# Kernel tuning notes

Measured on AMD Instinct MI355X. Metric: run time of the kernel, lower is better.

## Reference

```python
import jax, jax.numpy as jnp
import numpy as np

B, NP, DL, DA, H, NB = 8, 81920, 16, 4, 128, 3
DT_TOTAL = DL + DA  # 20
NSTEPS = 4
DT = 0.1


def setup_inputs() -> dict:
    key = jax.random.key(0)
    k1, k2, k3, k4 = jax.random.split(key, 4)
    inputs = jax.random.normal(k1, (B, NP, DT_TOTAL), dtype=jnp.float32)
    neighbours = jax.random.randint(k2, (NP, NB), 0, NP, dtype=jnp.int64)
    fan_in = NB * DT_TOTAL  # 60
    W1 = jax.random.normal(k3, (fan_in, H), dtype=jnp.float32) / np.sqrt(fan_in)
    b1 = jnp.zeros((H,), dtype=jnp.float32)
    W2 = jax.random.normal(k4, (H, DL), dtype=jnp.float32) / np.sqrt(H)
    b2 = jnp.zeros((DL,), dtype=jnp.float32)
    return {"inputs": inputs, "neighbours": neighbours, "W1": W1, "b1": b1, "W2": W2, "b2": b2}


def reference(inputs, neighbours, W1, b1, W2, b2):
    """nsteps of forward Euler: Y[..., :DL] += dt * Phi(gather(Y, neighbours))."""
    Y = inputs
    for _ in range(NSTEPS):
        # neighbour gather: (B, NP, NB, DT_TOTAL)
        Z = Y[:, neighbours, :]
        # shared interaction MLP on flattened neighbourhood features
        Zf = Z.reshape(B, NP, NB * DT_TOTAL)
        h = jnp.tanh(jnp.einsum('bpf,fh->bph', Zf, W1) + b1)
        fZ = jnp.einsum('bph,hd->bpd', h, W2) + b2  # (B, NP, DL)
        # pad with zeros over ancillary dims == update only latent slice
        Y = Y.at[..., :DL].add(DT * fZ)
    return Y
```

## Files before the change

### kernel.cpp

```cpp
#include <hip/hip_runtime.h>

#define B_DIM   8
#define NPTS    81920
#define DTOT    20
#define DT_STEP 0.1f

#define BLOCK 64
#define GRID  10240
#define ITERS 4
#define MROW  40
#define NFRAG 21
#define SMEM_BYTES 8704
#define FIMG_BYTES 32768
#define TANH_SCALE 2.885390082f

typedef __attribute__((ext_vector_type(8))) short    short8;
typedef __attribute__((ext_vector_type(4))) float    f32x4;
typedef __attribute__((ext_vector_type(2))) unsigned u32x2;
typedef __attribute__((ext_vector_type(4))) unsigned u32x4;
typedef __attribute__((ext_vector_type(2))) short    short2v;

__device__ __forceinline__ unsigned short f2bf(float f) {
    unsigned u = __builtin_bit_cast(unsigned, f);
    u += 0x7FFFu + ((u >> 16) & 1u);
    return (unsigned short)(u >> 16);
}
#if __has_builtin(__builtin_amdgcn_cvt_pk_bf16_f32)
__device__ __forceinline__ unsigned pack2(float a, float b) {
    short2v p = __builtin_amdgcn_cvt_pk_bf16_f32(a, b);
    return __builtin_bit_cast(unsigned, p);
}
#else
__device__ __forceinline__ unsigned pack2(float a, float b) {
    return (unsigned)f2bf(a) | ((unsigned)f2bf(b) << 16);
}
#endif
__device__ __forceinline__ float tanh_folded(float a) {
    float e = __builtin_amdgcn_exp2f(a);
    float r = __builtin_amdgcn_rcpf(1.0f + e);
    return 1.0f - 2.0f * r;
}

__device__ __forceinline__ int feat_of(int ks, int q, int j) {
    if (ks == 0) {
        if (q == 0) return j;
        if (q == 1) return 8 + j;
        if (q == 2) return 20 + j;
        return (j < 4) ? 16 + j : 36 + (j - 4);
    }
    if (q == 0) return 28 + j;
    if (q == 1) return 40 + j;
    if (q == 2) return 48 + j;
    if (j < 4) return 56 + j;
    return (j == 4) ? 60 : 61;
}

__global__ __launch_bounds__(256) void build_mirror(
    const f32x4* __restrict__ in, u32x2* __restrict__ m0,
    u32x2* __restrict__ m1, f32x4* __restrict__ outF, int n4,
    const float* __restrict__ W1, const float* __restrict__ b1,
    const float* __restrict__ W2, const float* __restrict__ b2,
    char* __restrict__ img)
{
    const int i = blockIdx.x * 256 + threadIdx.x;
    if (i < n4) {
        f32x4 v = in[i];
        u32x2 o; o.x = pack2(v.x, v.y); o.y = pack2(v.z, v.w);
        m0[i] = o;
        if ((i % 5) == 4) {
            m1[i] = o;
            outF[i] = v;
        }
    }
    if (blockIdx.x == 0) {
        const int t = threadIdx.x, lane = t & 63, g = t >> 6;
        const int l15 = lane & 15, q = lane >> 4;
        for (int f = g; f < NFRAG; f += 4) {
            char* dst = img + (f * 64 + lane) * 16;
            if (f < 16) {
                const int nt = f >> 1, ks = f & 1, m = nt * 16 + l15;
                unsigned short v[8];
                #pragma unroll
                for (int j = 0; j < 8; j++) {
                    const int ft = feat_of(ks, q, j);
                    float x = (ft < 60) ? TANH_SCALE * W1[ft * 128 + m]
                                        : (ft == 60 ? TANH_SCALE * b1[m] : 0.0f);
                    v[j] = f2bf(x);
                }
                *(u32x4*)dst = *(const u32x4*)v;
            } else if (f < 20) {
                const int ks = f - 16;
                unsigned short v[8];
                #pragma unroll
                for (int j = 0; j < 8; j++) {
                    const int k = ks * 32 + q * 8 + j;
                    v[j] = f2bf(DT_STEP * W2[k * 16 + l15]);
                }
                *(u32x4*)dst = *(const u32x4*)v;
            } else {
                f32x4 a = { DT_STEP * b2[q * 4 + 0], DT_STEP * b2[q * 4 + 1],
                            DT_STEP * b2[q * 4 + 2], DT_STEP * b2[q * 4 + 3] };
                *(f32x4*)dst = a;
            }
        }
    }
}

__device__ __forceinline__ void gather3(
    const char* __restrict__ MinB, int nx0, int nx1, int nx2,
    int offA, int offB, bool selA, bool selB, bool q3,
    u32x4& A, u32x4& Bv, u32x2& C)
{
    const int iA = selA ? nx1 : nx0;
    const int iB = selB ? nx2 : nx1;
    A  = *(const u32x4*)(MinB + (size_t)iA * MROW + offA);
    Bv = *(const u32x4*)(MinB + (size_t)iB * MROW + offB);
    u32x2 c = { 0u, 0u };
    if (q3) c = *(const u32x2*)(MinB + (size_t)nx2 * MROW + 32);
    C = c;
}

__global__ __launch_bounds__(BLOCK) void neural_step(
    const float* __restrict__ Yin, float* __restrict__ Yout,
    const unsigned short* __restrict__ Min,
    unsigned short* __restrict__ Mout,
    const int* __restrict__ nbr, const char* __restrict__ img,
    const int inStride, const int outStride, const int writeMirror)
{
    __shared__ __align__(16) char smem[SMEM_BYTES];
    const int t = threadIdx.x, lane = t & 63;
    const int l15 = lane & 15, q = lane >> 4;
    const bool q3 = (q == 3);
    const bool selA = (q == 2), selB = (q == 1) || (q == 2);
    const int offA = (q == 1) ? 16 : (q3 ? 32 : 0);
    const int offB = (q == 1) ? 0  : (q3 ? 32 : 16);

    const int bk = blockIdx.x;
    const int bB = bk & 7;
    const int p0 = (bk >> 3) * (ITERS * 16) + l15;
    const size_t rowBase = (size_t)bB * NPTS;
    const char*  MinB  = (const char*)Min + (size_t)bB * NPTS * MROW;
    char*        MoutB = (char*)Mout      + (size_t)bB * NPTS * MROW;

    int nx0, nx1, nx2, ny0 = 0, ny1 = 0, ny2 = 0;
    u32x4 gA, gB, nA = {0,0,0,0}, nB = {0,0,0,0};
    u32x2 gC, nC = {0,0};
    f32x4 ownC, ownN = {0.f, 0.f, 0.f, 0.f};
    {
        const int* np = nbr + (size_t)p0 * 3;
        nx0 = np[0]; nx1 = np[1]; nx2 = np[2];
        gather3(MinB, nx0, nx1, nx2, offA, offB, selA, selB, q3, gA, gB, gC);
        ownC = __builtin_nontemporal_load(
            (const f32x4*)(Yin + (rowBase + p0) * inStride) + q);
        const int* np1 = nbr + (size_t)(p0 + 16) * 3;
        nx0 = np1[0]; nx1 = np1[1]; nx2 = np1[2];
    }

    const short8* frg = (const short8*)img;
    short8 B1f[8][2];
    #pragma unroll
    for (int nt = 0; nt < 8; nt++)
        #pragma unroll
        for (int ks = 0; ks < 2; ks++)
            B1f[nt][ks] = frg[(nt * 2 + ks) * 64 + lane];
    short8 W2f[4];
    #pragma unroll
    for (int ks = 0; ks < 4; ks++)
        W2f[ks] = frg[(16 + ks) * 64 + lane];
    const f32x4 acc2init = ((const f32x4*)img)[20 * 64 + lane];

    #pragma unroll
    for (int it = 0; it < ITERS; it++) {
        unsigned short* hrow =
            (unsigned short*)(smem + (it & 1) * 4352);

        if (it + 1 < ITERS) {
            ownN = __builtin_nontemporal_load(
                (const f32x4*)(Yin + (rowBase + p0 + (it + 1) * 16) * inStride) + q);
            gather3(MinB, nx0, nx1, nx2, offA, offB, selA, selB, q3,
                    nA, nB, nC);
        }
        if (it + 2 < ITERS) {
            const int* np = nbr + (size_t)(p0 + (it + 2) * 16) * 3;
            ny0 = np[0]; ny1 = np[1]; ny2 = np[2];
        }

        u32x4 u0 = { gA.x, gA.y, q3 ? gB.x : gA.z, q3 ? gB.y : gA.w };
        u32x4 u1 = { q3 ? gC.x : gB.x, q3 ? gC.y : gB.y,
                     q3 ? 0x00003F80u : gB.z, q3 ? 0u : gB.w };
        short8 zb0 = __builtin_bit_cast(short8, u0);
        short8 zb1 = __builtin_bit_cast(short8, u1);

        #pragma unroll
        for (int nt = 0; nt < 8; nt++) {
            f32x4 acc = { 0.f, 0.f, 0.f, 0.f };
            acc = __builtin_amdgcn_mfma_f32_16x16x32_bf16(B1f[nt][0], zb0, acc, 0, 0, 0);
            acc = __builtin_amdgcn_mfma_f32_16x16x32_bf16(B1f[nt][1], zb1, acc, 0, 0, 0);
            u32x2 hw;
            hw.x = pack2(tanh_folded(acc[0]), tanh_folded(acc[1]));
            hw.y = pack2(tanh_folded(acc[2]), tanh_folded(acc[3]));
            *(u32x2*)((char*)hrow + l15 * 272 + nt * 32 + q * 8) = hw;
        }

        f32x4 acc2 = acc2init;
        #pragma unroll
        for (int ks = 0; ks < 4; ks++) {
            short8 hb = *(const short8*)((const char*)hrow + l15 * 272 + ks * 64 + q * 16);
            acc2 = __builtin_amdgcn_mfma_f32_16x16x32_bf16(W2f[ks], hb, acc2, 0, 0, 0);
        }

        const size_t row = rowBase + (size_t)(p0 + it * 16);
        f32x4 o = ownC;
        o.x += acc2[0]; o.y += acc2[1]; o.z += acc2[2]; o.w += acc2[3];
        *((f32x4*)(Yout + row * outStride) + q) = o;
        if (writeMirror) {
            char* mrow = MoutB + (size_t)(p0 + it * 16) * MROW;
            u32x2 mw; mw.x = pack2(o.x, o.y); mw.y = pack2(o.z, o.w);
            *(u32x2*)(mrow + q * 8) = mw;
        }

        ownC = ownN;
        gA = nA; gB = nB; gC = nC;
        nx0 = ny0; nx1 = ny1; nx2 = ny2;
    }
}

extern "C" void kernel_launch(void* const* d_in, const int* in_sizes, int n_in,
                              void* d_out, int out_size, void* d_ws, size_t ws_size,
                              hipStream_t stream) {
    const float* inputs = (const float*)d_in[0];
    const int*   nbr    = (const int*)  d_in[1];
    const float* W1     = (const float*)d_in[2];
    const float* b1     = (const float*)d_in[3];
    const float* W2     = (const float*)d_in[4];
    const float* b2     = (const float*)d_in[5];
    float* out = (float*)d_out;

    const size_t MBYTES = (size_t)B_DIM * NPTS * MROW;
    const size_t PBYTES = (size_t)B_DIM * NPTS * 16 * 4;
    unsigned short* M0 = (unsigned short*)d_ws;
    unsigned short* M1 = (unsigned short*)((char*)d_ws + MBYTES);
    char*           FI = (char*)d_ws + 2 * MBYTES;
    float*          P  = (float*)(FI + FIMG_BYTES);

    const bool usePacked = ws_size >= 2 * MBYTES + FIMG_BYTES + PBYTES;
    float* mid  = usePacked ? P : out;
    const int sMid = usePacked ? 16 : DTOT;

    const int n4 = B_DIM * NPTS * DTOT / 4;
    build_mirror<<<n4 / 256, 256, 0, stream>>>(
        (const f32x4*)inputs, (u32x2*)M0, (u32x2*)M1, (f32x4*)out, n4,
        W1, b1, W2, b2, FI);

    const dim3 grid(GRID), block(BLOCK);
    neural_step<<<grid, block, 0, stream>>>(inputs, mid, M0, M1, nbr, FI,
                                            DTOT, sMid, 1);
    neural_step<<<grid, block, 0, stream>>>(mid, mid, M1, M0, nbr, FI,
                                            sMid, sMid, 1);
    neural_step<<<grid, block, 0, stream>>>(mid, mid, M0, M1, nbr, FI,
                                            sMid, sMid, 1);
    neural_step<<<grid, block, 0, stream>>>(mid, out, M1, M0, nbr, FI,
                                            sMid, DTOT, 0);
}
```

Measured before the change: 285.1 us.

## Deepen gather prefetch pipeline to two stages and double points per block

Each block now processes 8 tiles of 16 points instead of 4, halving the grid, and the neighbour gather plus own-row loads are issued two iterations ahead instead of one, with neighbour indices read four iterations ahead. The goal is to hide more global gather latency and spread the per-block weight-fragment loads over more work. Launch bounds request 4 waves per SIMD to keep register use in check. This costs more live registers, and the smaller grid gives fewer blocks for latency hiding.

```diff
diff --git a/kernel.cpp b/kernel.cpp
--- a/kernel.cpp
+++ b/kernel.cpp
@@ -6,8 +6,8 @@
 #define DT_STEP 0.1f
 
 #define BLOCK 64
-#define GRID  10240
-#define ITERS 4
+#define GRID  5120
+#define ITERS 8
 #define MROW  40
 #define NFRAG 21
 #define SMEM_BYTES 8704
@@ -120,7 +120,7 @@
     C = c;
 }
 
-__global__ __launch_bounds__(BLOCK) void neural_step(
+__global__ __launch_bounds__(BLOCK, 4) void neural_step(
     const float* __restrict__ Yin, float* __restrict__ Yout,
     const unsigned short* __restrict__ Min,
     unsigned short* __restrict__ Mout,
@@ -142,18 +142,27 @@
     const char*  MinB  = (const char*)Min + (size_t)bB * NPTS * MROW;
     char*        MoutB = (char*)Mout      + (size_t)bB * NPTS * MROW;
 
-    int nx0, nx1, nx2, ny0 = 0, ny1 = 0, ny2 = 0;
-    u32x4 gA, gB, nA = {0,0,0,0}, nB = {0,0,0,0};
-    u32x2 gC, nC = {0,0};
-    f32x4 ownC, ownN = {0.f, 0.f, 0.f, 0.f};
+    u32x4 gA0, gB0, gA1, gB1, gA2 = {0,0,0,0}, gB2 = {0,0,0,0};
+    u32x2 gC0, gC1, gC2 = {0,0};
+    f32x4 own0, own1, own2 = {0.f, 0.f, 0.f, 0.f};
+    int nxA0, nxA1, nxA2;
+    int nxB0 = 0, nxB1 = 0, nxB2 = 0;
+
     {
-        const int* np = nbr + (size_t)p0 * 3;
-        nx0 = np[0]; nx1 = np[1]; nx2 = np[2];
-        gather3(MinB, nx0, nx1, nx2, offA, offB, selA, selB, q3, gA, gB, gC);
-        ownC = __builtin_nontemporal_load(
+        const int* np0 = nbr + (size_t)p0 * 3;
+        int a0 = np0[0], a1 = np0[1], a2 = np0[2];
+        gather3(MinB, a0, a1, a2, offA, offB, selA, selB, q3, gA0, gB0, gC0);
+        own0 = __builtin_nontemporal_load(
             (const f32x4*)(Yin + (rowBase + p0) * inStride) + q);
         const int* np1 = nbr + (size_t)(p0 + 16) * 3;
-        nx0 = np1[0]; nx1 = np1[1]; nx2 = np1[2];
+        int b0 = np1[0], b1i = np1[1], b2i = np1[2];
+        gather3(MinB, b0, b1i, b2i, offA, offB, selA, selB, q3, gA1, gB1, gC1);
+        own1 = __builtin_nontemporal_load(
+            (const f32x4*)(Yin + (rowBase + p0 + 16) * inStride) + q);
+        const int* np2 = nbr + (size_t)(p0 + 32) * 3;
+        nxA0 = np2[0]; nxA1 = np2[1]; nxA2 = np2[2];
+        const int* np3 = nbr + (size_t)(p0 + 48) * 3;
+        nxB0 = np3[0]; nxB1 = np3[1]; nxB2 = np3[2];
     }
 
     const short8* frg = (const short8*)img;
@@ -171,23 +180,25 @@
 
     #pragma unroll
     for (int it = 0; it < ITERS; it++) {
-        unsigned short* hrow =
-            (unsigned short*)(smem + (it & 1) * 4352);
-
-        if (it + 1 < ITERS) {
-            ownN = __builtin_nontemporal_load(
-                (const f32x4*)(Yin + (rowBase + p0 + (it + 1) * 16) * inStride) + q);
-            gather3(MinB, nx0, nx1, nx2, offA, offB, selA, selB, q3,
-                    nA, nB, nC);
-        }
+        unsigned short* hrow = (unsigned short*)(smem + (it & 1) * 4352);
+
         if (it + 2 < ITERS) {
-            const int* np = nbr + (size_t)(p0 + (it + 2) * 16) * 3;
-            ny0 = np[0]; ny1 = np[1]; ny2 = np[2];
-        }
-
-        u32x4 u0 = { gA.x, gA.y, q3 ? gB.x : gA.z, q3 ? gB.y : gA.w };
-        u32x4 u1 = { q3 ? gC.x : gB.x, q3 ? gC.y : gB.y,
-                     q3 ? 0x00003F80u : gB.z, q3 ? 0u : gB.w };
+            gather3(MinB, nxA0, nxA1, nxA2, offA, offB, selA, selB, q3,
+                    gA2, gB2, gC2);
+            own2 = __builtin_nontemporal_load(
+                (const f32x4*)(Yin + (rowBase + p0 + (it + 2) * 16) * inStride) + q);
+        }
+        if (it + 4 < ITERS) {
+            const int* np = nbr + (size_t)(p0 + (it + 4) * 16) * 3;
+            nxA0 = nxB0; nxA1 = nxB1; nxA2 = nxB2;
+            nxB0 = np[0]; nxB1 = np[1]; nxB2 = np[2];
+        } else {
+            nxA0 = nxB0; nxA1 = nxB1; nxA2 = nxB2;
+        }
+
+        u32x4 u0 = { gA0.x, gA0.y, q3 ? gB0.x : gA0.z, q3 ? gB0.y : gA0.w };
+        u32x4 u1 = { q3 ? gC0.x : gB0.x, q3 ? gC0.y : gB0.y,
+                     q3 ? 0x00003F80u : gB0.z, q3 ? 0u : gB0.w };
         short8 zb0 = __builtin_bit_cast(short8, u0);
         short8 zb1 = __builtin_bit_cast(short8, u1);
 
@@ -210,7 +221,7 @@
         }
 
         const size_t row = rowBase + (size_t)(p0 + it * 16);
-        f32x4 o = ownC;
+        f32x4 o = own0;
         o.x += acc2[0]; o.y += acc2[1]; o.z += acc2[2]; o.w += acc2[3];
         *((f32x4*)(Yout + row * outStride) + q) = o;
         if (writeMirror) {
@@ -219,9 +230,9 @@
             *(u32x2*)(mrow + q * 8) = mw;
         }
 
-        ownC = ownN;
-        gA = nA; gB = nB; gC = nC;
-        nx0 = ny0; nx1 = ny1; nx2 = ny2;
+        own0 = own1; own1 = own2;
+        gA0 = gA1; gB0 = gB1; gC0 = gC1;
+        gA1 = gA2; gB1 = gB2; gC1 = gC2;
     }
 }
 
```

Measured after the change: 547.8 us. 92.2% more time.
